# Kernel optimization log

Measured on AMD Instinct MI355X. Metric: run time of the kernel, lower is better.

The kernel has to match this reference:

```python
import jax, jax.numpy as jnp
import numpy as np

B, T, J, D = 32, 1024, 64, 256


def setup_inputs() -> dict:
    key = jax.random.key(0)
    k1, k2, k3, k4 = jax.random.split(key, 4)
    U = jax.random.normal(k1, (B, J, D), dtype=jnp.float32)
    H = jax.random.normal(k2, (B, T, D), dtype=jnp.float32)
    # similarity_layer: Linear(3*D, 1) -> weight [3*D], bias scalar
    w = jax.random.normal(k3, (3 * D,), dtype=jnp.float32) * (1.0 / np.sqrt(3 * D))
    b = jax.random.normal(k4, (), dtype=jnp.float32) * 0.01
    return {"U": U, "H": H, "w": w, "b": b}


def reference(U, H, w, b):
    # Linear([H; U; H*U]) decomposes exactly into three small contractions:
    # S[b,t,j] = H[b,t]@w_h + U[b,j]@w_u + (H[b,t]*w_hu)@U[b,j] + bias
    w_h, w_u, w_hu = w[:D], w[D:2 * D], w[2 * D:]
    S = (
        jnp.einsum("btd,d->bt", H, w_h)[:, :, None]
        + jnp.einsum("bjd,d->bj", U, w_u)[:, None, :]
        + jnp.einsum("btd,bjd->btj", H * w_hu, U)
        + b
    )  # [B, T, J]
    A = jax.nn.softmax(S, axis=2)                      # context-to-query attention
    c2q = jnp.einsum("btj,bjd->btd", A, U)             # [B, T, D]
    b_att = jax.nn.softmax(jnp.max(S, axis=2), axis=1)  # [B, T]
    q2c = jnp.einsum("bt,btd->bd", b_att, H)[:, None, :]  # [B, 1, D]
    G = jnp.concatenate((H, c2q, H * c2q, H * q2c), axis=2)  # [B, T, 4D]
    return (G, c2q, q2c)
```

## Files before the change

### kernel.cpp

```cpp
#include <hip/hip_runtime.h>
#include <hip/hip_bf16.h>

#define BB 32
#define TT 1024
#define JJ 64
#define DD 256

__device__ __forceinline__ float wave_sum64(float v) {
    #pragma unroll
    for (int m = 32; m >= 1; m >>= 1) v += __shfl_xor(v, m, 64);
    return v;
}
__device__ __forceinline__ float wave_max64(float v) {
    #pragma unroll
    for (int m = 32; m >= 1; m >>= 1) v = fmaxf(v, __shfl_xor(v, m, 64));
    return v;
}

__global__ __launch_bounds__(256) void k0_prep(const float* __restrict__ U,
                                               const float* __restrict__ w,
                                               const float* __restrict__ bp,
                                               float* __restrict__ Up,
                                               float* __restrict__ uw) {
    int wave = threadIdx.x >> 6;
    int lane = threadIdx.x & 63;
    int row  = blockIdx.x * 4 + wave;
    const float* ur = U + (size_t)row * DD + lane * 4;
    float4 u   = *(const float4*)ur;
    float4 whu = *(const float4*)(w + 2 * DD + lane * 4);
    float4 wu  = *(const float4*)(w + DD + lane * 4);
    float4 o;
    o.x = u.x * whu.x; o.y = u.y * whu.y; o.z = u.z * whu.z; o.w = u.w * whu.w;
    *(float4*)(Up + (size_t)row * DD + lane * 4) = o;
    float p = fmaf(u.x, wu.x, fmaf(u.y, wu.y, fmaf(u.z, wu.z, u.w * wu.w)));
    p = wave_sum64(p);
    if (lane == 0) uw[row] = p + bp[0];
}

__global__ __launch_bounds__(256, 2) void k1_main(const float* __restrict__ H,
                                                  const float* __restrict__ U,
                                                  const float* __restrict__ Up,
                                                  const float* __restrict__ uw,
                                                  const float* __restrict__ w,
                                                  float* __restrict__ m_ws,
                                                  float* __restrict__ G,
                                                  float* __restrict__ c2q_out) {
    __shared__ float lds[20480];
    const int tid  = threadIdx.x;
    const int lane = tid & 63;
    const int wave = __builtin_amdgcn_readfirstlane(tid >> 6);
    const int b    = blockIdx.x >> 4;
    const int t0   = (blockIdx.x & 15) << 6;

    const float* Ub = Up + (size_t)b * JJ * DD;
    #pragma unroll
    for (int it = 0; it < 16; ++it) {
        int lin = it * 256 + tid;
        int j   = lin >> 6;
        int dcc = lin & 63;
        float4 v = *(const float4*)(Ub + (size_t)j * DD + dcc * 4);
        int byteoff = j * 1024 + ((dcc * 16) ^ ((j & 7) << 4));
        *(float4*)((char*)lds + byteoff) = v;
    }
    __syncthreads();

    const float uwj = uw[b * JJ + lane];
    const float wh0 = w[lane], wh1 = w[64 + lane], wh2 = w[128 + lane], wh3 = w[192 + lane];
    const int   swz = (lane & 7) << 4;
    const char* urow = (const char*)lds + lane * 1024;
    const float* Hb  = H + (size_t)b * TT * DD;

    #pragma unroll 1
    for (int rg = 0; rg < 4; ++rg) {
        const int r0 = t0 + wave * 16 + rg * 4;
        const float* h0 = Hb + (size_t)(r0 + 0) * DD;
        const float* h1 = Hb + (size_t)(r0 + 1) * DD;
        const float* h2 = Hb + (size_t)(r0 + 2) * DD;
        const float* h3 = Hb + (size_t)(r0 + 3) * DD;
        float a0 = 0.f, a1 = 0.f, a2 = 0.f, a3 = 0.f;
        #pragma unroll 4
        for (int dc = 0; dc < 64; ++dc) {
            float4 u  = *(const float4*)(urow + ((dc * 16) ^ swz));
            float4 x0 = *(const float4*)(h0 + dc * 4);
            float4 x1 = *(const float4*)(h1 + dc * 4);
            float4 x2 = *(const float4*)(h2 + dc * 4);
            float4 x3 = *(const float4*)(h3 + dc * 4);
            a0 = fmaf(x0.x, u.x, fmaf(x0.y, u.y, fmaf(x0.z, u.z, fmaf(x0.w, u.w, a0))));
            a1 = fmaf(x1.x, u.x, fmaf(x1.y, u.y, fmaf(x1.z, u.z, fmaf(x1.w, u.w, a1))));
            a2 = fmaf(x2.x, u.x, fmaf(x2.y, u.y, fmaf(x2.z, u.z, fmaf(x2.w, u.w, a2))));
            a3 = fmaf(x3.x, u.x, fmaf(x3.y, u.y, fmaf(x3.z, u.z, fmaf(x3.w, u.w, a3))));
        }
        float sv[4] = {a0, a1, a2, a3};
        #pragma unroll
        for (int i = 0; i < 4; ++i) {
            const int row = r0 + i;
            const float* hr = Hb + (size_t)row * DD;
            float hwp = fmaf(hr[lane], wh0,
                        fmaf(hr[64 + lane], wh1,
                        fmaf(hr[128 + lane], wh2, hr[192 + lane] * wh3)));
            float hw = wave_sum64(hwp);
            float s  = sv[i] + uwj;
            float mx = wave_max64(s);
            float p  = __expf(s - mx);
            float l  = wave_sum64(p);
            lds[16384 + (wave * 16 + rg * 4 + i) * 64 + lane] = p * (1.0f / l);
            if (lane == 0) m_ws[b * TT + row] = mx + hw;
        }
    }
    __syncthreads();

    const float* Ug = U + (size_t)b * JJ * DD;
    #pragma unroll
    for (int it = 0; it < 16; ++it) {
        int lin = it * 256 + tid;
        int j   = lin >> 6;
        int dcc = lin & 63;
        float4 v = *(const float4*)(Ug + (size_t)j * DD + dcc * 4);
        int byteoff = j * 1024 + ((dcc * 16) ^ ((j & 7) << 4));
        *(float4*)((char*)lds + byteoff) = v;
    }
    __syncthreads();

    float4 acc[16];
    #pragma unroll
    for (int r = 0; r < 16; ++r) { acc[r].x = 0.f; acc[r].y = 0.f; acc[r].z = 0.f; acc[r].w = 0.f; }
    const float* Arow = &lds[16384 + (wave * 16) * 64];
    #pragma unroll 4
    for (int j = 0; j < 64; ++j) {
        float4 u = *(const float4*)((const char*)lds + j * 1024 + ((lane * 16) ^ ((j & 7) << 4)));
        #pragma unroll
        for (int r = 0; r < 16; ++r) {
            float aj = Arow[r * 64 + j];
            acc[r].x = fmaf(aj, u.x, acc[r].x);
            acc[r].y = fmaf(aj, u.y, acc[r].y);
            acc[r].z = fmaf(aj, u.z, acc[r].z);
            acc[r].w = fmaf(aj, u.w, acc[r].w);
        }
    }

    const size_t Gbase = (size_t)b * TT * 1024;
    #pragma unroll 1
    for (int r = 0; r < 16; ++r) {
        const int row = t0 + wave * 16 + r;
        float4 h4 = *(const float4*)(Hb + (size_t)row * DD + lane * 4);
        float4 c  = acc[r];
        float4 hc;
        hc.x = h4.x * c.x; hc.y = h4.y * c.y; hc.z = h4.z * c.z; hc.w = h4.w * c.w;
        float* Grow = G + Gbase + (size_t)row * 1024;
        *(float4*)(Grow + lane * 4)        = h4;
        *(float4*)(Grow + 256 + lane * 4)  = c;
        *(float4*)(Grow + 512 + lane * 4)  = hc;
        *(float4*)(c2q_out + ((size_t)b * TT + row) * DD + lane * 4) = c;
    }
}

__global__ __launch_bounds__(256) void k2_batt(const float* __restrict__ m_ws,
                                               float* __restrict__ wt,
                                               float* __restrict__ q2c_out) {
    __shared__ float red[256];
    const int b = blockIdx.x, tid = threadIdx.x;
    float v0 = m_ws[b * TT + tid];
    float v1 = m_ws[b * TT + 256 + tid];
    float v2 = m_ws[b * TT + 512 + tid];
    float v3 = m_ws[b * TT + 768 + tid];
    red[tid] = fmaxf(fmaxf(v0, v1), fmaxf(v2, v3));
    __syncthreads();
    for (int s = 128; s >= 1; s >>= 1) {
        if (tid < s) red[tid] = fmaxf(red[tid], red[tid + s]);
        __syncthreads();
    }
    const float M = red[0];
    __syncthreads();
    float e0 = __expf(v0 - M), e1 = __expf(v1 - M), e2 = __expf(v2 - M), e3 = __expf(v3 - M);
    red[tid] = e0 + e1 + e2 + e3;
    __syncthreads();
    for (int s = 128; s >= 1; s >>= 1) {
        if (tid < s) red[tid] += red[tid + s];
        __syncthreads();
    }
    const float iz = 1.0f / red[0];
    wt[b * TT + tid]       = e0 * iz;
    wt[b * TT + 256 + tid] = e1 * iz;
    wt[b * TT + 512 + tid] = e2 * iz;
    wt[b * TT + 768 + tid] = e3 * iz;
    q2c_out[b * DD + tid] = 0.0f;
}

__global__ __launch_bounds__(256) void k2b_q2c(const float* __restrict__ H,
                                               const float* __restrict__ wt,
                                               float* __restrict__ q2c_out) {
    const int b = blockIdx.x >> 3, c = blockIdx.x & 7, tid = threadIdx.x;
    const float* Hb = H + ((size_t)b * TT + c * 128) * DD;
    const float* wb = wt + b * TT + c * 128;
    float acc = 0.f;
    #pragma unroll 4
    for (int i = 0; i < 128; ++i) acc = fmaf(wb[i], Hb[(size_t)i * DD + tid], acc);
    atomicAdd(&q2c_out[b * DD + tid], acc);
}

__global__ __launch_bounds__(256) void k3_gtail(const float* __restrict__ H,
                                                const float* __restrict__ q2c,
                                                float* __restrict__ G) {
    const size_t idx = (size_t)blockIdx.x * 256 + threadIdx.x;
    const int d4 = (int)(idx & 63);
    const size_t bt = idx >> 6;
    const int b = (int)(bt >> 10);
    float4 h = *(const float4*)(H + idx * 4);
    float4 q = *(const float4*)(q2c + (size_t)b * DD + d4 * 4);
    float4 o;
    o.x = h.x * q.x; o.y = h.y * q.y; o.z = h.z * q.z; o.w = h.w * q.w;
    *(float4*)(G + bt * 1024 + 768 + d4 * 4) = o;
}

extern "C" void kernel_launch(void* const* d_in, const int* in_sizes, int n_in,
                              void* d_out, int out_size, void* d_ws, size_t ws_size,
                              hipStream_t stream) {
    const float* U  = (const float*)d_in[0];
    const float* H  = (const float*)d_in[1];
    const float* w  = (const float*)d_in[2];
    const float* bp = (const float*)d_in[3];
    float* out = (float*)d_out;

    float* G       = out;
    float* c2q_out = out + (size_t)BB * TT * 4 * DD;
    float* q2c_out = c2q_out + (size_t)BB * TT * DD;

    float* Up   = (float*)d_ws;
    float* uwp  = Up + (size_t)BB * JJ * DD;
    float* m_ws = uwp + BB * JJ;
    float* wtp  = m_ws + BB * TT;

    k0_prep<<<BB * JJ / 4, 256, 0, stream>>>(U, w, bp, Up, uwp);
    k1_main<<<BB * (TT / 64), 256, 0, stream>>>(H, U, Up, uwp, w, m_ws, G, c2q_out);
    k2_batt<<<BB, 256, 0, stream>>>(m_ws, wtp, q2c_out);
    k2b_q2c<<<BB * 8, 256, 0, stream>>>(H, wtp, q2c_out);
    k3_gtail<<<BB * TT * DD / 4 / 256, 256, 0, stream>>>(H, q2c_out, G);
}
```

Before: 298.4 us.

## Widen main kernel to 8 waves, move H·w_h to prep kernel, batch reductions

k1_main now runs 512 threads per block, with each wave handling 8 rows in one pass instead of 16 rows over four groups. The per-row H·w_h dot product moves out of it into the prep kernel, which gains extra blocks to compute it. Row softmax reductions are batched across 8 rows, and the U tile load into LDS is overlapped with the softmax so one barrier can go. The unswizzled U layout in the second phase may bring back LDS bank conflicts. k2b_q2c is split into more chunks, and higher register pressure may limit occupancy.

```diff
diff --git a/kernel.cpp b/kernel.cpp
--- a/kernel.cpp
+++ b/kernel.cpp
@@ -6,42 +6,53 @@
 #define JJ 64
 #define DD 256
 
-__device__ __forceinline__ float wave_sum64(float v) {
-    #pragma unroll
-    for (int m = 32; m >= 1; m >>= 1) v += __shfl_xor(v, m, 64);
-    return v;
-}
-__device__ __forceinline__ float wave_max64(float v) {
-    #pragma unroll
-    for (int m = 32; m >= 1; m >>= 1) v = fmaxf(v, __shfl_xor(v, m, 64));
-    return v;
-}
-
 __global__ __launch_bounds__(256) void k0_prep(const float* __restrict__ U,
+                                               const float* __restrict__ H,
                                                const float* __restrict__ w,
                                                const float* __restrict__ bp,
                                                float* __restrict__ Up,
-                                               float* __restrict__ uw) {
-    int wave = threadIdx.x >> 6;
-    int lane = threadIdx.x & 63;
-    int row  = blockIdx.x * 4 + wave;
-    const float* ur = U + (size_t)row * DD + lane * 4;
-    float4 u   = *(const float4*)ur;
-    float4 whu = *(const float4*)(w + 2 * DD + lane * 4);
-    float4 wu  = *(const float4*)(w + DD + lane * 4);
-    float4 o;
-    o.x = u.x * whu.x; o.y = u.y * whu.y; o.z = u.z * whu.z; o.w = u.w * whu.w;
-    *(float4*)(Up + (size_t)row * DD + lane * 4) = o;
-    float p = fmaf(u.x, wu.x, fmaf(u.y, wu.y, fmaf(u.z, wu.z, u.w * wu.w)));
-    p = wave_sum64(p);
-    if (lane == 0) uw[row] = p + bp[0];
-}
-
-__global__ __launch_bounds__(256, 2) void k1_main(const float* __restrict__ H,
+                                               float* __restrict__ uw,
+                                               float* __restrict__ hw) {
+    const int wave = threadIdx.x >> 6;
+    const int lane = threadIdx.x & 63;
+    if (blockIdx.x < 512) {
+        const int row = blockIdx.x * 4 + wave;
+        float4 u   = *(const float4*)(U + (size_t)row * DD + lane * 4);
+        float4 whu = *(const float4*)(w + 2 * DD + lane * 4);
+        float4 wu  = *(const float4*)(w + DD + lane * 4);
+        float4 o;
+        o.x = u.x * whu.x; o.y = u.y * whu.y; o.z = u.z * whu.z; o.w = u.w * whu.w;
+        *(float4*)(Up + (size_t)row * DD + lane * 4) = o;
+        float p = fmaf(u.x, wu.x, fmaf(u.y, wu.y, fmaf(u.z, wu.z, u.w * wu.w)));
+        #pragma unroll
+        for (int m = 32; m >= 1; m >>= 1) p += __shfl_xor(p, m, 64);
+        if (lane == 0) uw[row] = p + bp[0];
+    } else {
+        const int base = (blockIdx.x - 512) * 64 + wave * 16;
+        float4 wh = *(const float4*)(w + lane * 4);
+        float pr[16];
+        #pragma unroll
+        for (int r = 0; r < 16; ++r) {
+            float4 h = *(const float4*)(H + (size_t)(base + r) * DD + lane * 4);
+            pr[r] = fmaf(h.x, wh.x, fmaf(h.y, wh.y, fmaf(h.z, wh.z, h.w * wh.w)));
+        }
+        #pragma unroll
+        for (int m = 32; m >= 1; m >>= 1) {
+            #pragma unroll
+            for (int r = 0; r < 16; ++r) pr[r] += __shfl_xor(pr[r], m, 64);
+        }
+        if (lane == 0) {
+            #pragma unroll
+            for (int r = 0; r < 16; ++r) hw[base + r] = pr[r];
+        }
+    }
+}
+
+__global__ __launch_bounds__(512, 4) void k1_main(const float* __restrict__ H,
                                                   const float* __restrict__ U,
                                                   const float* __restrict__ Up,
                                                   const float* __restrict__ uw,
-                                                  const float* __restrict__ w,
+                                                  const float* __restrict__ hw,
                                                   float* __restrict__ m_ws,
                                                   float* __restrict__ G,
                                                   float* __restrict__ c2q_out) {
@@ -51,86 +62,104 @@
     const int wave = __builtin_amdgcn_readfirstlane(tid >> 6);
     const int b    = blockIdx.x >> 4;
     const int t0   = (blockIdx.x & 15) << 6;
+    const int r0   = t0 + wave * 8;
 
     const float* Ub = Up + (size_t)b * JJ * DD;
     #pragma unroll
-    for (int it = 0; it < 16; ++it) {
-        int lin = it * 256 + tid;
-        int j   = lin >> 6;
-        int dcc = lin & 63;
-        float4 v = *(const float4*)(Ub + (size_t)j * DD + dcc * 4);
-        int byteoff = j * 1024 + ((dcc * 16) ^ ((j & 7) << 4));
-        *(float4*)((char*)lds + byteoff) = v;
+    for (int it = 0; it < 8; ++it) {
+        const int j = it * 8 + wave;
+        float4 v = *(const float4*)((const char*)Ub + j * 1024 + lane * 16);
+        *(float4*)((char*)lds + j * 1024 + ((lane * 16) ^ ((j & 7) << 4))) = v;
     }
     __syncthreads();
 
     const float uwj = uw[b * JJ + lane];
-    const float wh0 = w[lane], wh1 = w[64 + lane], wh2 = w[128 + lane], wh3 = w[192 + lane];
     const int   swz = (lane & 7) << 4;
     const char* urow = (const char*)lds + lane * 1024;
     const float* Hb  = H + (size_t)b * TT * DD;
 
-    #pragma unroll 1
-    for (int rg = 0; rg < 4; ++rg) {
-        const int r0 = t0 + wave * 16 + rg * 4;
-        const float* h0 = Hb + (size_t)(r0 + 0) * DD;
-        const float* h1 = Hb + (size_t)(r0 + 1) * DD;
-        const float* h2 = Hb + (size_t)(r0 + 2) * DD;
-        const float* h3 = Hb + (size_t)(r0 + 3) * DD;
-        float a0 = 0.f, a1 = 0.f, a2 = 0.f, a3 = 0.f;
-        #pragma unroll 4
-        for (int dc = 0; dc < 64; ++dc) {
-            float4 u  = *(const float4*)(urow + ((dc * 16) ^ swz));
-            float4 x0 = *(const float4*)(h0 + dc * 4);
-            float4 x1 = *(const float4*)(h1 + dc * 4);
-            float4 x2 = *(const float4*)(h2 + dc * 4);
-            float4 x3 = *(const float4*)(h3 + dc * 4);
-            a0 = fmaf(x0.x, u.x, fmaf(x0.y, u.y, fmaf(x0.z, u.z, fmaf(x0.w, u.w, a0))));
-            a1 = fmaf(x1.x, u.x, fmaf(x1.y, u.y, fmaf(x1.z, u.z, fmaf(x1.w, u.w, a1))));
-            a2 = fmaf(x2.x, u.x, fmaf(x2.y, u.y, fmaf(x2.z, u.z, fmaf(x2.w, u.w, a2))));
-            a3 = fmaf(x3.x, u.x, fmaf(x3.y, u.y, fmaf(x3.z, u.z, fmaf(x3.w, u.w, a3))));
-        }
-        float sv[4] = {a0, a1, a2, a3};
-        #pragma unroll
-        for (int i = 0; i < 4; ++i) {
-            const int row = r0 + i;
-            const float* hr = Hb + (size_t)row * DD;
-            float hwp = fmaf(hr[lane], wh0,
-                        fmaf(hr[64 + lane], wh1,
-                        fmaf(hr[128 + lane], wh2, hr[192 + lane] * wh3)));
-            float hw = wave_sum64(hwp);
-            float s  = sv[i] + uwj;
-            float mx = wave_max64(s);
-            float p  = __expf(s - mx);
-            float l  = wave_sum64(p);
-            lds[16384 + (wave * 16 + rg * 4 + i) * 64 + lane] = p * (1.0f / l);
-            if (lane == 0) m_ws[b * TT + row] = mx + hw;
-        }
+    const float* h0 = Hb + (size_t)(r0 + 0) * DD;
+    const float* h1 = Hb + (size_t)(r0 + 1) * DD;
+    const float* h2 = Hb + (size_t)(r0 + 2) * DD;
+    const float* h3 = Hb + (size_t)(r0 + 3) * DD;
+    const float* h4p = Hb + (size_t)(r0 + 4) * DD;
+    const float* h5 = Hb + (size_t)(r0 + 5) * DD;
+    const float* h6 = Hb + (size_t)(r0 + 6) * DD;
+    const float* h7 = Hb + (size_t)(r0 + 7) * DD;
+    float a0 = 0.f, a1 = 0.f, a2 = 0.f, a3 = 0.f, a4 = 0.f, a5 = 0.f, a6 = 0.f, a7 = 0.f;
+    #pragma unroll 2
+    for (int dc = 0; dc < 64; ++dc) {
+        float4 u  = *(const float4*)(urow + ((dc * 16) ^ swz));
+        float4 x0 = *(const float4*)(h0 + dc * 4);
+        float4 x1 = *(const float4*)(h1 + dc * 4);
+        float4 x2 = *(const float4*)(h2 + dc * 4);
+        float4 x3 = *(const float4*)(h3 + dc * 4);
+        float4 x4 = *(const float4*)(h4p + dc * 4);
+        float4 x5 = *(const float4*)(h5 + dc * 4);
+        float4 x6 = *(const float4*)(h6 + dc * 4);
+        float4 x7 = *(const float4*)(h7 + dc * 4);
+        a0 = fmaf(x0.x, u.x, fmaf(x0.y, u.y, fmaf(x0.z, u.z, fmaf(x0.w, u.w, a0))));
+        a1 = fmaf(x1.x, u.x, fmaf(x1.y, u.y, fmaf(x1.z, u.z, fmaf(x1.w, u.w, a1))));
+        a2 = fmaf(x2.x, u.x, fmaf(x2.y, u.y, fmaf(x2.z, u.z, fmaf(x2.w, u.w, a2))));
+        a3 = fmaf(x3.x, u.x, fmaf(x3.y, u.y, fmaf(x3.z, u.z, fmaf(x3.w, u.w, a3))));
+        a4 = fmaf(x4.x, u.x, fmaf(x4.y, u.y, fmaf(x4.z, u.z, fmaf(x4.w, u.w, a4))));
+        a5 = fmaf(x5.x, u.x, fmaf(x5.y, u.y, fmaf(x5.z, u.z, fmaf(x5.w, u.w, a5))));
+        a6 = fmaf(x6.x, u.x, fmaf(x6.y, u.y, fmaf(x6.z, u.z, fmaf(x6.w, u.w, a6))));
+        a7 = fmaf(x7.x, u.x, fmaf(x7.y, u.y, fmaf(x7.z, u.z, fmaf(x7.w, u.w, a7))));
     }
     __syncthreads();
 
     const float* Ug = U + (size_t)b * JJ * DD;
-    #pragma unroll
-    for (int it = 0; it < 16; ++it) {
-        int lin = it * 256 + tid;
-        int j   = lin >> 6;
-        int dcc = lin & 63;
-        float4 v = *(const float4*)(Ug + (size_t)j * DD + dcc * 4);
-        int byteoff = j * 1024 + ((dcc * 16) ^ ((j & 7) << 4));
-        *(float4*)((char*)lds + byteoff) = v;
-    }
-    __syncthreads();
-
-    float4 acc[16];
-    #pragma unroll
-    for (int r = 0; r < 16; ++r) { acc[r].x = 0.f; acc[r].y = 0.f; acc[r].z = 0.f; acc[r].w = 0.f; }
-    const float* Arow = &lds[16384 + (wave * 16) * 64];
-    #pragma unroll 4
+    float4 st[8];
+    #pragma unroll
+    for (int it = 0; it < 8; ++it) {
+        const int j = it * 8 + wave;
+        st[it] = *(const float4*)((const char*)Ug + j * 1024 + lane * 16);
+    }
+
+    float s[8] = {a0 + uwj, a1 + uwj, a2 + uwj, a3 + uwj,
+                  a4 + uwj, a5 + uwj, a6 + uwj, a7 + uwj};
+    float mx[8];
+    #pragma unroll
+    for (int r = 0; r < 8; ++r) mx[r] = s[r];
+    #pragma unroll
+    for (int m = 32; m >= 1; m >>= 1) {
+        #pragma unroll
+        for (int r = 0; r < 8; ++r) mx[r] = fmaxf(mx[r], __shfl_xor(mx[r], m, 64));
+    }
+    float p[8], l[8];
+    #pragma unroll
+    for (int r = 0; r < 8; ++r) { p[r] = __expf(s[r] - mx[r]); l[r] = p[r]; }
+    #pragma unroll
+    for (int m = 32; m >= 1; m >>= 1) {
+        #pragma unroll
+        for (int r = 0; r < 8; ++r) l[r] += __shfl_xor(l[r], m, 64);
+    }
+    #pragma unroll
+    for (int r = 0; r < 8; ++r)
+        lds[16384 + (wave * 8 + r) * 64 + lane] = p[r] * (1.0f / l[r]);
+    if (lane == 0) {
+        #pragma unroll
+        for (int r = 0; r < 8; ++r) m_ws[b * TT + r0 + r] = mx[r] + hw[b * TT + r0 + r];
+    }
+
+    #pragma unroll
+    for (int it = 0; it < 8; ++it) {
+        const int j = it * 8 + wave;
+        *(float4*)((char*)lds + j * 1024 + lane * 16) = st[it];
+    }
+    __syncthreads();
+
+    float4 acc[8];
+    #pragma unroll
+    for (int r = 0; r < 8; ++r) { acc[r].x = 0.f; acc[r].y = 0.f; acc[r].z = 0.f; acc[r].w = 0.f; }
+    const float* Arow = &lds[16384 + (wave * 8) * 64];
+    #pragma unroll 2
     for (int j = 0; j < 64; ++j) {
-        float4 u = *(const float4*)((const char*)lds + j * 1024 + ((lane * 16) ^ ((j & 7) << 4)));
-        #pragma unroll
-        for (int r = 0; r < 16; ++r) {
-            float aj = Arow[r * 64 + j];
+        float4 u = *(const float4*)((const char*)lds + j * 1024 + lane * 16);
+        #pragma unroll
+        for (int r = 0; r < 8; ++r) {
+            const float aj = Arow[r * 64 + j];
             acc[r].x = fmaf(aj, u.x, acc[r].x);
             acc[r].y = fmaf(aj, u.y, acc[r].y);
             acc[r].z = fmaf(aj, u.z, acc[r].z);
@@ -140,8 +169,8 @@
 
     const size_t Gbase = (size_t)b * TT * 1024;
     #pragma unroll 1
-    for (int r = 0; r < 16; ++r) {
-        const int row = t0 + wave * 16 + r;
+    for (int r = 0; r < 8; ++r) {
+        const int row = r0 + r;
         float4 h4 = *(const float4*)(Hb + (size_t)row * DD + lane * 4);
         float4 c  = acc[r];
         float4 hc;
@@ -189,12 +218,12 @@
 __global__ __launch_bounds__(256) void k2b_q2c(const float* __restrict__ H,
                                                const float* __restrict__ wt,
                                                float* __restrict__ q2c_out) {
-    const int b = blockIdx.x >> 3, c = blockIdx.x & 7, tid = threadIdx.x;
-    const float* Hb = H + ((size_t)b * TT + c * 128) * DD;
-    const float* wb = wt + b * TT + c * 128;
+    const int b = blockIdx.x >> 4, c = blockIdx.x & 15, tid = threadIdx.x;
+    const float* Hb = H + ((size_t)b * TT + c * 64) * DD;
+    const float* wb = wt + b * TT + c * 64;
     float acc = 0.f;
     #pragma unroll 4
-    for (int i = 0; i < 128; ++i) acc = fmaf(wb[i], Hb[(size_t)i * DD + tid], acc);
+    for (int i = 0; i < 64; ++i) acc = fmaf(wb[i], Hb[(size_t)i * DD + tid], acc);
     atomicAdd(&q2c_out[b * DD + tid], acc);
 }
 
@@ -229,10 +258,11 @@
     float* uwp  = Up + (size_t)BB * JJ * DD;
     float* m_ws = uwp + BB * JJ;
     float* wtp  = m_ws + BB * TT;
-
-    k0_prep<<<BB * JJ / 4, 256, 0, stream>>>(U, w, bp, Up, uwp);
-    k1_main<<<BB * (TT / 64), 256, 0, stream>>>(H, U, Up, uwp, w, m_ws, G, c2q_out);
+    float* hwp  = wtp + BB * TT;
+
+    k0_prep<<<1024, 256, 0, stream>>>(U, H, w, bp, Up, uwp, hwp);
+    k1_main<<<BB * (TT / 64), 512, 0, stream>>>(H, U, Up, uwp, hwp, m_ws, G, c2q_out);
     k2_batt<<<BB, 256, 0, stream>>>(m_ws, wtp, q2c_out);
-    k2b_q2c<<<BB * 8, 256, 0, stream>>>(H, wtp, q2c_out);
+    k2b_q2c<<<BB * 16, 256, 0, stream>>>(H, wtp, q2c_out);
     k3_gtail<<<BB * TT * DD / 4 / 256, 256, 0, stream>>>(H, q2c_out, G);
 }
```

After: 284.7 us. 1.05x faster.
